# Kernel optimization log

Measured on AMD Instinct MI355X. Metric: run time of the kernel, lower is better.

## Reference

```python
import jax, jax.numpy as jnp
import numpy as np

WS = 16            # window height = width
DIM = 512          # channels
H = 16             # num heads
HD = DIM // H      # head dim = 32
NW = 64            # num windows per image (mask leading dim)
B_ = 256           # num_windows * batch
N_IN = 512         # pre-stride sequence length
SCALE = HD ** -0.5
MAX_SEQ = 512
STRIDE = 2


def _relative_position_index(wh, ww):
    coords = np.stack(np.meshgrid(np.arange(wh), np.arange(ww), indexing='ij'))  # (2, wh, ww)
    cf = coords.reshape(2, -1)                             # (2, wh*ww)
    rc = (cf[:, :, None] - cf[:, None, :]).transpose(1, 2, 0).astype(np.int32)
    rc[:, :, 0] += wh - 1
    rc[:, :, 1] += ww - 1
    rc[:, :, 0] *= 2 * ww - 1
    return rc.sum(-1)                                      # (wh*ww, wh*ww)


def setup_inputs() -> dict:
    key = jax.random.key(0)
    ks = jax.random.split(key, 8)
    x = jax.random.normal(ks[0], (B_, N_IN, DIM), dtype=jnp.float32)
    y = jax.random.normal(ks[1], (B_, N_IN, DIM), dtype=jnp.float32)
    mask = jax.random.normal(ks[2], (NW, WS * WS, WS * WS), dtype=jnp.float32)
    q_w = jax.random.normal(ks[3], (DIM, DIM), dtype=jnp.float32) * 0.02
    q_b = jnp.zeros((DIM,), dtype=jnp.float32)
    kv_w = jax.random.normal(ks[4], (2 * DIM, DIM), dtype=jnp.float32) * 0.02
    kv_b = jnp.zeros((2 * DIM,), dtype=jnp.float32)
    proj_w = jax.random.normal(ks[5], (DIM, DIM), dtype=jnp.float32) * 0.02
    proj_b = jnp.zeros((DIM,), dtype=jnp.float32)
    bias_table = jax.random.normal(ks[6], ((2 * WS - 1) ** 2, H), dtype=jnp.float32) * 0.02
    rel_pos_index = jnp.asarray(_relative_position_index(WS, WS))  # (256, 256) int32
    return {"x": x, "y": y, "mask": mask, "q_w": q_w, "q_b": q_b,
            "kv_w": kv_w, "kv_b": kv_b, "proj_w": proj_w, "proj_b": proj_b,
            "bias_table": bias_table, "rel_pos_index": rel_pos_index}


def reference(x, y, mask, q_w, q_b, kv_w, kv_b, proj_w, proj_b, bias_table, rel_pos_index):
    # truncate + stride (as in forward)
    x = x[:, :MAX_SEQ][:, ::STRIDE]          # (B_, N, C), N = 256
    y = y[:, :MAX_SEQ][:, ::STRIDE]
    b, n, c = x.shape
    # projections
    q = (x @ q_w.T + q_b).reshape(b, n, H, HD).transpose(0, 2, 1, 3)   # (B_, H, N, D)
    kv = y @ kv_w.T + kv_b                                              # (B_, N, 2C)
    k = kv[..., :DIM].reshape(b, n, H, HD).transpose(0, 2, 1, 3)
    v = kv[..., DIM:].reshape(b, n, H, HD).transpose(0, 2, 1, 3)
    # scores
    attn = jnp.einsum('bhnd,bhmd->bhnm', q * SCALE, k)                  # (B_, H, N, N)
    # gathered relative position bias: (N, N, H) -> (H, N, N)
    rpb = bias_table[rel_pos_index].transpose(2, 0, 1)
    attn = attn + rpb[None]
    # window mask: view (B_//nW, nW, H, N, N) + mask[None,:,None]
    attn = attn.reshape(b // NW, NW, H, n, n) + mask[None, :, None]
    attn = attn.reshape(b, H, n, n)
    attn = jax.nn.softmax(attn, axis=-1)
    out = jnp.einsum('bhnm,bhmd->bhnd', attn, v)                        # (B_, H, N, D)
    out = out.transpose(0, 2, 1, 3).reshape(b, n, DIM)
    out = out @ proj_w.T + proj_b
    return out
```

## Files before the change

kernel.cpp:

```cpp
#include <hip/hip_runtime.h>

typedef _Float16 half8 __attribute__((ext_vector_type(8)));
typedef _Float16 half4 __attribute__((ext_vector_type(4)));
typedef _Float16 half2v __attribute__((ext_vector_type(2)));
typedef float f32x4 __attribute__((ext_vector_type(4)));

#define LOG2E 1.4426950408889634f
#define QSCALE (0.17677669529663687f * 1.4426950408889634f)

static __device__ __forceinline__ half4 cvt4h(float4 v) {
    half2v a = __builtin_bit_cast(half2v, __builtin_amdgcn_cvt_pkrtz(v.x, v.y));
    half2v b = __builtin_bit_cast(half2v, __builtin_amdgcn_cvt_pkrtz(v.z, v.w));
    return half4{ a[0], a[1], b[0], b[1] };
}

static __device__ __forceinline__ void gl16(const _Float16* g, _Float16* l) {
    __builtin_amdgcn_global_load_lds(
        (const __attribute__((address_space(1))) void*)g,
        (__attribute__((address_space(3))) void*)l, 16, 0, 0);
}

#define NB_X 16384
#define NB_Y 16384
#define NB_W 512
#define NB_M 4096
#define NB_R 4096

__global__ __launch_bounds__(256) void convert_kernel(
    const float* __restrict__ x, const float* __restrict__ y,
    const float* __restrict__ q_w, const float* __restrict__ kv_w,
    const float* __restrict__ proj_w, const float* __restrict__ mask,
    const float* __restrict__ table, const int* __restrict__ rpi,
    _Float16* __restrict__ Xh, _Float16* __restrict__ Yh,
    _Float16* __restrict__ Wh, _Float16* __restrict__ maskh,
    _Float16* __restrict__ rpbh)
{
    const int blk = blockIdx.x, t = threadIdx.x;
    if (blk < NB_X + NB_Y) {
        const float* src; _Float16* dst; int v;
        if (blk < NB_X) { v = blk * 256 + t; src = x; dst = Xh; }
        else { v = (blk - NB_X) * 256 + t; src = y; dst = Yh; }
        int r = v >> 6, ks = (v & 63) * 8;
        const float* s = src + ((size_t)(r >> 8) * 512 + (size_t)((r & 255) * 2)) * 512 + ks;
        half4 h0 = cvt4h(*(const float4*)s);
        half4 h1 = cvt4h(*(const float4*)(s + 4));
        half8 hv = { h0[0], h0[1], h0[2], h0[3], h1[0], h1[1], h1[2], h1[3] };
        *(half8*)(dst + (size_t)v * 8) = hv;
    } else if (blk < NB_X + NB_Y + NB_W) {
        int v = (blk - NB_X - NB_Y) * 256 + t;
        int row = v >> 6, ks = (v & 63) * 8;
        const float* s; float sc = 1.0f;
        if (row < 512)       { s = q_w + (size_t)row * 512;            sc = QSCALE; }
        else if (row < 1536) { s = kv_w + (size_t)(row - 512) * 512; }
        else                 { s = proj_w + (size_t)(row - 1536) * 512; }
        float4 a = *(const float4*)(s + ks);
        float4 b = *(const float4*)(s + ks + 4);
        a.x *= sc; a.y *= sc; a.z *= sc; a.w *= sc;
        b.x *= sc; b.y *= sc; b.z *= sc; b.w *= sc;
        half4 h0 = cvt4h(a), h1 = cvt4h(b);
        half8 hv = { h0[0], h0[1], h0[2], h0[3], h1[0], h1[1], h1[2], h1[3] };
        *(half8*)(Wh + (size_t)v * 8) = hv;
    } else if (blk < NB_X + NB_Y + NB_W + NB_M) {
        int i = (blk - NB_X - NB_Y - NB_W) * 256 + t;
        float4 v = ((const float4*)mask)[i];
        half4 hv = { (_Float16)(v.x * LOG2E), (_Float16)(v.y * LOG2E),
                     (_Float16)(v.z * LOG2E), (_Float16)(v.w * LOG2E) };
        *(half4*)(maskh + (size_t)i * 4) = hv;
    } else {
        int i = (blk - NB_X - NB_Y - NB_W - NB_M) * 256 + t;
        int p = i & 65535, hh = i >> 16;
        rpbh[i] = (_Float16)(table[rpi[p] * 16 + hh] * LOG2E);
    }
}

__global__ __launch_bounds__(256) void gemm_f16(
    const _Float16* __restrict__ Ah, const _Float16* __restrict__ Wh,
    const float* __restrict__ bias, float bscale,
    _Float16* __restrict__ qout, _Float16* __restrict__ kout,
    _Float16* __restrict__ vout, float* __restrict__ fout,
    int mode, int nct_sh)
{
    __shared__ __align__(16) _Float16 As[128 * 64];
    __shared__ __align__(16) _Float16 Ws[128 * 64];
    const int nwg = gridDim.x;
    const int chunk = nwg >> 3;
    const int f = blockIdx.x;
    const int swz = (f & 7) * chunk + (f >> 3);
    const int ct = swz & ((1 << nct_sh) - 1);
    const int rt = swz >> nct_sh;

    const int t = threadIdx.x;
    const int lane = t & 63, wave = t >> 6;
    const int ql = lane & 15, g = lane >> 4;
    const int wr = (wave >> 1) * 64, wc = (wave & 1) * 64;

    const int lr = lane >> 3;
    const int ls = (lane & 7) ^ lr;
    const _Float16* aB = Ah + ((size_t)(rt * 128 + wave * 8 + lr)) * 512 + ls * 8;
    const _Float16* wB = Wh + ((size_t)(ct * 128 + wave * 8 + lr)) * 512 + ls * 8;
    _Float16* asW = As + wave * 8 * 64;
    _Float16* wsW = Ws + wave * 8 * 64;

    f32x4 acc[4][4] = {};
    for (int kk = 0; kk < 8; ++kk) {
        const int k0 = kk * 64;
        if (kk) __syncthreads();
#pragma unroll
        for (int p = 0; p < 4; ++p) {
            gl16(aB + (size_t)p * 32 * 512 + k0, asW + p * 32 * 64);
            gl16(wB + (size_t)p * 32 * 512 + k0, wsW + p * 32 * 64);
        }
        __syncthreads();
#pragma unroll
        for (int kh = 0; kh < 2; ++kh) {
            half8 af[4], bf[4];
#pragma unroll
            for (int i = 0; i < 4; ++i) {
                int row = wr + i * 16 + ql;
                af[i] = *(const half8*)((const char*)As + row * 128 +
                        (((kh * 4 + g) ^ (ql & 7)) << 4));
            }
#pragma unroll
            for (int j = 0; j < 4; ++j) {
                int row = wc + j * 16 + ql;
                bf[j] = *(const half8*)((const char*)Ws + row * 128 +
                        (((kh * 4 + g) ^ (ql & 7)) << 4));
            }
#pragma unroll
            for (int i = 0; i < 4; ++i)
#pragma unroll
                for (int j = 0; j < 4; ++j)
                    acc[i][j] = __builtin_amdgcn_mfma_f32_16x16x32_f16(af[i], bf[j], acc[i][j], 0, 0, 0);
        }
    }

#pragma unroll
    for (int j = 0; j < 4; ++j) {
        int c = ct * 128 + wc + j * 16 + ql;
        float bv = bias[c] * bscale;
#pragma unroll
        for (int i = 0; i < 4; ++i) {
#pragma unroll
            for (int rr = 0; rr < 4; ++rr) {
                int r = rt * 128 + wr + i * 16 + g * 4 + rr;
                float val = acc[i][j][rr] + bv;
                if (mode == 2) {
                    fout[(size_t)r * 512 + c] = val;
                } else {
                    _Float16 hv = (_Float16)val;
                    int b = r >> 8, n = r & 255;
                    if (mode == 0) {
                        int hh = c >> 5, d = c & 31;
                        qout[((size_t)(b * 16 + hh) * 256 + n) * 32 + d] = hv;
                    } else if (c < 512) {
                        int hh = c >> 5, d = c & 31;
                        kout[((size_t)(b * 16 + hh) * 256 + n) * 32 + d] = hv;
                    } else {
                        int c2 = c - 512, hh = c2 >> 5, d = c2 & 31;
                        vout[((size_t)(b * 16 + hh) * 256 + n) * 32 + d] = hv;
                    }
                }
            }
        }
    }
}

__global__ __launch_bounds__(256, 2) void attn_kernel(
    const _Float16* __restrict__ Q, const _Float16* __restrict__ K,
    const _Float16* __restrict__ V, const _Float16* __restrict__ rpbh,
    const _Float16* __restrict__ maskh, _Float16* __restrict__ pre)
{
    __shared__ __align__(16) _Float16 bias_s[2][16 * 256];
    const int blk = blockIdx.x;
    const int w = blk >> 4, h = blk & 15;
    const int t = threadIdx.x;
    const int lane = t & 63, wave = t >> 6;
    const int ql = lane & 15, g = lane >> 4;
    const int b = w + 64 * wave;
    const size_t blk_b = (size_t)(b * 16 + h) * 8192;
    const _Float16* Qp = Q + blk_b + g * 8;
    const _Float16* Kp = K + blk_b + ql * 32 + g * 8;
    const _Float16* rp = rpbh + (size_t)h * 65536;
    const _Float16* mp = maskh + (size_t)w * 65536;

    half8 karr[16];
#pragma unroll
    for (int tt = 0; tt < 16; ++tt)
        karr[tt] = *(const half8*)(Kp + tt * 512);

    half4 vf0[16], vf1[16];
    {
        const _Float16* vb = V + blk_b + g * 128 + ql;
#pragma unroll
        for (int tt = 0; tt < 16; ++tt) {
#pragma unroll
            for (int j = 0; j < 4; ++j) {
                vf0[tt][j] = vb[tt * 512 + j * 32];
                vf1[tt][j] = vb[tt * 512 + j * 32 + 16];
            }
        }
    }

    const int sq = t >> 4;
    const int scb = (t & 15) * 32;
    const int sw = sq << 3;
    const int sgoff = (t & 15) * 16;

    {
        const _Float16* rrow = rp + (size_t)sq * 256 + sgoff;
        const _Float16* mrow = mp + (size_t)sq * 256 + sgoff;
        half8 s0 = *(const half8*)rrow + *(const half8*)mrow;
        half8 s1 = *(const half8*)(rrow + 8) + *(const half8*)(mrow + 8);
        char* sb = (char*)bias_s[0] + sq * 512;
        *(half4*)(sb + ((scb) ^ sw))      = __builtin_shufflevector(s0, s0, 0, 1, 2, 3);
        *(half4*)(sb + ((scb + 8) ^ sw))  = __builtin_shufflevector(s0, s0, 4, 5, 6, 7);
        *(half4*)(sb + ((scb + 16) ^ sw)) = __builtin_shufflevector(s1, s1, 0, 1, 2, 3);
        *(half4*)(sb + ((scb + 24) ^ sw)) = __builtin_shufflevector(s1, s1, 4, 5, 6, 7);
    }
    __syncthreads();

#pragma unroll 1
    for (int qg = 0; qg < 16; ++qg) {
        const int q0 = qg * 16;
        half8 nr0, nm0, nr1, nm1;
        if (qg < 15) {
            const _Float16* rrow = rp + (size_t)(q0 + 16 + sq) * 256 + sgoff;
            const _Float16* mrow = mp + (size_t)(q0 + 16 + sq) * 256 + sgoff;
            nr0 = *(const half8*)rrow;
            nm0 = *(const half8*)mrow;
            nr1 = *(const half8*)(rrow + 8);
            nm1 = *(const half8*)(mrow + 8);
        }

        const int q = q0 + ql;
        half8 qf = *(const half8*)(Qp + (size_t)q * 32);
        const char* bb = (const char*)bias_s[qg & 1] + ql * 512;
        f32x4 lsum = { 0.f, 0.f, 0.f, 0.f };
        f32x4 o0 = { 0.f, 0.f, 0.f, 0.f }, o1 = { 0.f, 0.f, 0.f, 0.f };
#pragma unroll
        for (int tt = 0; tt < 16; ++tt) {
            half4 bs = *(const half4*)(bb + ((tt * 32 + g * 8) ^ (ql << 3)));
            f32x4 bf = { (float)bs[0], (float)bs[1], (float)bs[2], (float)bs[3] };
            f32x4 s = __builtin_amdgcn_mfma_f32_16x16x32_f16(karr[tt], qf, bf, 0, 0, 0);
            float e0 = __builtin_amdgcn_exp2f(s[0]);
            float e1 = __builtin_amdgcn_exp2f(s[1]);
            float e2 = __builtin_amdgcn_exp2f(s[2]);
            float e3 = __builtin_amdgcn_exp2f(s[3]);
            lsum[0] += e0; lsum[1] += e1; lsum[2] += e2; lsum[3] += e3;
            half2v p01 = __builtin_bit_cast(half2v, __builtin_amdgcn_cvt_pkrtz(e0, e1));
            half2v p23 = __builtin_bit_cast(half2v, __builtin_amdgcn_cvt_pkrtz(e2, e3));
            half4 pf = { p01[0], p01[1], p23[0], p23[1] };
            o0 = __builtin_amdgcn_mfma_f32_16x16x16f16(pf, vf0[tt], o0, 0, 0, 0);
            o1 = __builtin_amdgcn_mfma_f32_16x16x16f16(pf, vf1[tt], o1, 0, 0, 0);
        }
        float l = (lsum[0] + lsum[1]) + (lsum[2] + lsum[3]);
        l += __shfl_xor(l, 16);
        l += __shfl_xor(l, 32);
#pragma unroll
        for (int rr = 0; rr < 4; ++rr) {
            float inv = __builtin_amdgcn_rcpf(__shfl(l, g * 4 + rr));
            int row = q0 + g * 4 + rr;
            size_t ob = ((size_t)b * 256 + row) * 512 + h * 32;
            pre[ob + ql] = (_Float16)(o0[rr] * inv);
            pre[ob + 16 + ql] = (_Float16)(o1[rr] * inv);
        }
        if (qg < 15) {
            half8 s0 = nr0 + nm0, s1 = nr1 + nm1;
            char* sb = (char*)bias_s[(qg + 1) & 1] + sq * 512;
            *(half4*)(sb + ((scb) ^ sw))      = __builtin_shufflevector(s0, s0, 0, 1, 2, 3);
            *(half4*)(sb + ((scb + 8) ^ sw))  = __builtin_shufflevector(s0, s0, 4, 5, 6, 7);
            *(half4*)(sb + ((scb + 16) ^ sw)) = __builtin_shufflevector(s1, s1, 0, 1, 2, 3);
            *(half4*)(sb + ((scb + 24) ^ sw)) = __builtin_shufflevector(s1, s1, 4, 5, 6, 7);
        }
        __syncthreads();
    }
}

extern "C" void kernel_launch(void* const* d_in, const int* in_sizes, int n_in,
                              void* d_out, int out_size, void* d_ws, size_t ws_size,
                              hipStream_t stream)
{
    const float* x      = (const float*)d_in[0];
    const float* y      = (const float*)d_in[1];
    const float* mask   = (const float*)d_in[2];
    const float* q_w    = (const float*)d_in[3];
    const float* q_b    = (const float*)d_in[4];
    const float* kv_w   = (const float*)d_in[5];
    const float* kv_b   = (const float*)d_in[6];
    const float* proj_w = (const float*)d_in[7];
    const float* proj_b = (const float*)d_in[8];
    const float* btab   = (const float*)d_in[9];
    const int*   rpi    = (const int*)d_in[10];
    float* out = (float*)d_out;

    char* ws = (char*)d_ws;
    _Float16* XK  = (_Float16*)(ws);
    _Float16* YP  = (_Float16*)(ws + ((size_t)64 << 20));
    _Float16* Qw  = (_Float16*)(ws + ((size_t)128 << 20));
    _Float16* Vw  = (_Float16*)(ws + ((size_t)192 << 20));
    _Float16* Wh  = (_Float16*)(ws + ((size_t)256 << 20));
    _Float16* Rpb = (_Float16*)(ws + ((size_t)258 << 20));
    _Float16* Mh  = (_Float16*)(ws + ((size_t)260 << 20));

    convert_kernel<<<NB_X + NB_Y + NB_W + NB_M + NB_R, 256, 0, stream>>>(
        x, y, q_w, kv_w, proj_w, mask, btab, rpi, XK, YP, Wh, Mh, Rpb);
    gemm_f16<<<2048, 256, 0, stream>>>(XK, Wh, q_b, QSCALE,
                                       Qw, nullptr, nullptr, nullptr, 0, 2);
    gemm_f16<<<4096, 256, 0, stream>>>(YP, Wh + 512 * 512, kv_b, 1.0f,
                                       nullptr, XK, Vw, nullptr, 1, 3);
    attn_kernel<<<1024, 256, 0, stream>>>(Qw, XK, Vw, Rpb, Mh, YP);
    gemm_f16<<<2048, 256, 0, stream>>>(YP, Wh + 1536 * 512, proj_b, 1.0f,
                                       nullptr, nullptr, nullptr, out, 2, 2);
}
```

Measured before the change: 497.0 us.

## Fuse fp32-to-fp16 activation conversion into projection GEMM tile loads

Removes the standalone conversion pass over x and y and has the Q and KV projection GEMMs load fp32 strided rows directly, converting to fp16 in registers before storing to LDS. Global-to-LDS direct loads are replaced by a register-prefetch pipeline that loads the next K-slice while computing the current one. This removes an intermediate fp16 write and re-read, at the cost of reading wider fp32 data per column tile and more register pressure.

```diff
diff --git a/kernel.cpp b/kernel.cpp
--- a/kernel.cpp
+++ b/kernel.cpp
@@ -14,40 +14,20 @@
     return half4{ a[0], a[1], b[0], b[1] };
 }
 
-static __device__ __forceinline__ void gl16(const _Float16* g, _Float16* l) {
-    __builtin_amdgcn_global_load_lds(
-        (const __attribute__((address_space(1))) void*)g,
-        (__attribute__((address_space(3))) void*)l, 16, 0, 0);
-}
-
-#define NB_X 16384
-#define NB_Y 16384
-#define NB_W 512
-#define NB_M 4096
-#define NB_R 4096
-
-__global__ __launch_bounds__(256) void convert_kernel(
-    const float* __restrict__ x, const float* __restrict__ y,
+#define PB_W 512
+#define PB_M 4096
+#define PB_R 4096
+
+__global__ __launch_bounds__(256) void prep_kernel(
     const float* __restrict__ q_w, const float* __restrict__ kv_w,
     const float* __restrict__ proj_w, const float* __restrict__ mask,
     const float* __restrict__ table, const int* __restrict__ rpi,
-    _Float16* __restrict__ Xh, _Float16* __restrict__ Yh,
     _Float16* __restrict__ Wh, _Float16* __restrict__ maskh,
     _Float16* __restrict__ rpbh)
 {
     const int blk = blockIdx.x, t = threadIdx.x;
-    if (blk < NB_X + NB_Y) {
-        const float* src; _Float16* dst; int v;
-        if (blk < NB_X) { v = blk * 256 + t; src = x; dst = Xh; }
-        else { v = (blk - NB_X) * 256 + t; src = y; dst = Yh; }
-        int r = v >> 6, ks = (v & 63) * 8;
-        const float* s = src + ((size_t)(r >> 8) * 512 + (size_t)((r & 255) * 2)) * 512 + ks;
-        half4 h0 = cvt4h(*(const float4*)s);
-        half4 h1 = cvt4h(*(const float4*)(s + 4));
-        half8 hv = { h0[0], h0[1], h0[2], h0[3], h1[0], h1[1], h1[2], h1[3] };
-        *(half8*)(dst + (size_t)v * 8) = hv;
-    } else if (blk < NB_X + NB_Y + NB_W) {
-        int v = (blk - NB_X - NB_Y) * 256 + t;
+    if (blk < PB_W) {
+        int v = blk * 256 + t;
         int row = v >> 6, ks = (v & 63) * 8;
         const float* s; float sc = 1.0f;
         if (row < 512)       { s = q_w + (size_t)row * 512;            sc = QSCALE; }
@@ -60,23 +40,24 @@
         half4 h0 = cvt4h(a), h1 = cvt4h(b);
         half8 hv = { h0[0], h0[1], h0[2], h0[3], h1[0], h1[1], h1[2], h1[3] };
         *(half8*)(Wh + (size_t)v * 8) = hv;
-    } else if (blk < NB_X + NB_Y + NB_W + NB_M) {
-        int i = (blk - NB_X - NB_Y - NB_W) * 256 + t;
+    } else if (blk < PB_W + PB_M) {
+        int i = (blk - PB_W) * 256 + t;
         float4 v = ((const float4*)mask)[i];
         half4 hv = { (_Float16)(v.x * LOG2E), (_Float16)(v.y * LOG2E),
                      (_Float16)(v.z * LOG2E), (_Float16)(v.w * LOG2E) };
         *(half4*)(maskh + (size_t)i * 4) = hv;
     } else {
-        int i = (blk - NB_X - NB_Y - NB_W - NB_M) * 256 + t;
+        int i = (blk - PB_W - PB_M) * 256 + t;
         int p = i & 65535, hh = i >> 16;
         rpbh[i] = (_Float16)(table[rpi[p] * 16 + hh] * LOG2E);
     }
 }
 
-__global__ __launch_bounds__(256) void gemm_f16(
-    const _Float16* __restrict__ Ah, const _Float16* __restrict__ Wh,
-    const float* __restrict__ bias, float bscale,
-    _Float16* __restrict__ qout, _Float16* __restrict__ kout,
+template<bool F32A>
+static __device__ __forceinline__ void gemm_core(
+    const float* __restrict__ Af, const _Float16* __restrict__ Ah,
+    const _Float16* __restrict__ Wh, const float* __restrict__ bias,
+    float bscale, _Float16* __restrict__ qout, _Float16* __restrict__ kout,
     _Float16* __restrict__ vout, float* __restrict__ fout,
     int mode, int nct_sh)
 {
@@ -94,23 +75,64 @@
     const int ql = lane & 15, g = lane >> 4;
     const int wr = (wave >> 1) * 64, wc = (wave & 1) * 64;
 
-    const int lr = lane >> 3;
-    const int ls = (lane & 7) ^ lr;
-    const _Float16* aB = Ah + ((size_t)(rt * 128 + wave * 8 + lr)) * 512 + ls * 8;
-    const _Float16* wB = Wh + ((size_t)(ct * 128 + wave * 8 + lr)) * 512 + ls * 8;
-    _Float16* asW = As + wave * 8 * 64;
-    _Float16* wsW = Ws + wave * 8 * 64;
+    const int sr = t >> 3;
+    const int st = t & 7;
+    const float* aFp[4];
+    const _Float16* aHp[4];
+#pragma unroll
+    for (int p = 0; p < 4; ++p) {
+        int r = rt * 128 + sr + p * 32;
+        if constexpr (F32A)
+            aFp[p] = Af + ((size_t)(r >> 8) * 512 + (size_t)((r & 255) * 2)) * 512 + st * 8;
+        else
+            aHp[p] = Ah + (size_t)r * 512 + st * 8;
+    }
+    const _Float16* wR = Wh + ((size_t)(ct * 128 + sr)) * 512 + st * 8;
+    char* asw = (char*)As + sr * 128 + ((st ^ (sr & 7)) << 4);
+    char* wsw = (char*)Ws + sr * 128 + ((st ^ (sr & 7)) << 4);
+
+    float4 alo[4], ahi[4];
+    half8 aS[4], wS[4];
+#pragma unroll
+    for (int p = 0; p < 4; ++p) {
+        if constexpr (F32A) {
+            alo[p] = *(const float4*)(aFp[p]);
+            ahi[p] = *(const float4*)(aFp[p] + 4);
+        } else {
+            aS[p] = *(const half8*)(aHp[p]);
+        }
+        wS[p] = *(const half8*)(wR + p * 32 * 512);
+    }
 
     f32x4 acc[4][4] = {};
     for (int kk = 0; kk < 8; ++kk) {
-        const int k0 = kk * 64;
         if (kk) __syncthreads();
 #pragma unroll
         for (int p = 0; p < 4; ++p) {
-            gl16(aB + (size_t)p * 32 * 512 + k0, asW + p * 32 * 64);
-            gl16(wB + (size_t)p * 32 * 512 + k0, wsW + p * 32 * 64);
+            half8 av;
+            if constexpr (F32A) {
+                half4 l = cvt4h(alo[p]), h = cvt4h(ahi[p]);
+                av = half8{ l[0], l[1], l[2], l[3], h[0], h[1], h[2], h[3] };
+            } else {
+                av = aS[p];
+            }
+            *(half8*)(asw + p * 4096) = av;
+            *(half8*)(wsw + p * 4096) = wS[p];
         }
         __syncthreads();
+        if (kk < 7) {
+            const int k0n = (kk + 1) * 64;
+#pragma unroll
+            for (int p = 0; p < 4; ++p) {
+                if constexpr (F32A) {
+                    alo[p] = *(const float4*)(aFp[p] + k0n);
+                    ahi[p] = *(const float4*)(aFp[p] + k0n + 4);
+                } else {
+                    aS[p] = *(const half8*)(aHp[p] + k0n);
+                }
+                wS[p] = *(const half8*)(wR + p * 32 * 512 + k0n);
+            }
+        }
 #pragma unroll
         for (int kh = 0; kh < 2; ++kh) {
             half8 af[4], bf[4];
@@ -165,6 +187,24 @@
     }
 }
 
+__global__ __launch_bounds__(256) void gemm_f32a(
+    const float* __restrict__ Af, const _Float16* __restrict__ Wh,
+    const float* __restrict__ bias, float bscale,
+    _Float16* __restrict__ qout, _Float16* __restrict__ kout,
+    _Float16* __restrict__ vout, int mode, int nct_sh)
+{
+    gemm_core<true>(Af, nullptr, Wh, bias, bscale, qout, kout, vout,
+                    nullptr, mode, nct_sh);
+}
+
+__global__ __launch_bounds__(256) void gemm_f16a(
+    const _Float16* __restrict__ Ah, const _Float16* __restrict__ Wh,
+    const float* __restrict__ bias, float* __restrict__ fout, int nct_sh)
+{
+    gemm_core<false>(nullptr, Ah, Wh, bias, 1.0f, nullptr, nullptr, nullptr,
+                     fout, 2, nct_sh);
+}
+
 __global__ __launch_bounds__(256, 2) void attn_kernel(
     const _Float16* __restrict__ Q, const _Float16* __restrict__ K,
     const _Float16* __restrict__ V, const _Float16* __restrict__ rpbh,
@@ -294,21 +334,20 @@
     float* out = (float*)d_out;
 
     char* ws = (char*)d_ws;
-    _Float16* XK  = (_Float16*)(ws);
-    _Float16* YP  = (_Float16*)(ws + ((size_t)64 << 20));
-    _Float16* Qw  = (_Float16*)(ws + ((size_t)128 << 20));
-    _Float16* Vw  = (_Float16*)(ws + ((size_t)192 << 20));
+    _Float16* Qw  = (_Float16*)(ws);
+    _Float16* Kw  = (_Float16*)(ws + ((size_t)64 << 20));
+    _Float16* Vw  = (_Float16*)(ws + ((size_t)128 << 20));
+    _Float16* Pre = (_Float16*)(ws + ((size_t)192 << 20));
     _Float16* Wh  = (_Float16*)(ws + ((size_t)256 << 20));
     _Float16* Rpb = (_Float16*)(ws + ((size_t)258 << 20));
     _Float16* Mh  = (_Float16*)(ws + ((size_t)260 << 20));
 
-    convert_kernel<<<NB_X + NB_Y + NB_W + NB_M + NB_R, 256, 0, stream>>>(
-        x, y, q_w, kv_w, proj_w, mask, btab, rpi, XK, YP, Wh, Mh, Rpb);
-    gemm_f16<<<2048, 256, 0, stream>>>(XK, Wh, q_b, QSCALE,
-                                       Qw, nullptr, nullptr, nullptr, 0, 2);
-    gemm_f16<<<4096, 256, 0, stream>>>(YP, Wh + 512 * 512, kv_b, 1.0f,
-                                       nullptr, XK, Vw, nullptr, 1, 3);
-    attn_kernel<<<1024, 256, 0, stream>>>(Qw, XK, Vw, Rpb, Mh, YP);
-    gemm_f16<<<2048, 256, 0, stream>>>(YP, Wh + 1536 * 512, proj_b, 1.0f,
-                                       nullptr, nullptr, nullptr, out, 2, 2);
-}
+    prep_kernel<<<PB_W + PB_M + PB_R, 256, 0, stream>>>(
+        q_w, kv_w, proj_w, mask, btab, rpi, Wh, Mh, Rpb);
+    gemm_f32a<<<2048, 256, 0, stream>>>(x, Wh, q_b, QSCALE,
+                                        Qw, nullptr, nullptr, 0, 2);
+    gemm_f32a<<<4096, 256, 0, stream>>>(y, Wh + 512 * 512, kv_b, 1.0f,
+                                        nullptr, Kw, Vw, 1, 3);
+    attn_kernel<<<1024, 256, 0, stream>>>(Qw, Kw, Vw, Rpb, Mh, Pre);
+    gemm_f16a<<<2048, 256, 0, stream>>>(Pre, Wh + 1536 * 512, proj_b, out, 2);
+}
```

After: 484.5 us. 2.5% less time.

## Load GEMM operands directly from global memory into registers, dropping LDS staging

Applied to the files above, without the earlier changes.

The f16 GEMM no longer stages A and W tiles through shared memory with global_load_lds and two barriers per k-step. Each lane now reads its MFMA fragments straight from global memory, and the k-loop is fully unrolled. This removes LDS traffic and synchronization, but gives up the sharing of tiles between waves. Each A and W element is now fetched from global/L2 by two waves, and the reads are strided 16-byte loads that depend on cache hits.

```diff
diff --git a/kernel.cpp b/kernel.cpp
--- a/kernel.cpp
+++ b/kernel.cpp
@@ -12,12 +12,6 @@
     half2v a = __builtin_bit_cast(half2v, __builtin_amdgcn_cvt_pkrtz(v.x, v.y));
     half2v b = __builtin_bit_cast(half2v, __builtin_amdgcn_cvt_pkrtz(v.z, v.w));
     return half4{ a[0], a[1], b[0], b[1] };
-}
-
-static __device__ __forceinline__ void gl16(const _Float16* g, _Float16* l) {
-    __builtin_amdgcn_global_load_lds(
-        (const __attribute__((address_space(1))) void*)g,
-        (__attribute__((address_space(3))) void*)l, 16, 0, 0);
 }
 
 #define NB_X 16384
@@ -80,8 +74,6 @@
     _Float16* __restrict__ vout, float* __restrict__ fout,
     int mode, int nct_sh)
 {
-    __shared__ __align__(16) _Float16 As[128 * 64];
-    __shared__ __align__(16) _Float16 Ws[128 * 64];
     const int nwg = gridDim.x;
     const int chunk = nwg >> 3;
     const int f = blockIdx.x;
@@ -94,38 +86,22 @@
     const int ql = lane & 15, g = lane >> 4;
     const int wr = (wave >> 1) * 64, wc = (wave & 1) * 64;
 
-    const int lr = lane >> 3;
-    const int ls = (lane & 7) ^ lr;
-    const _Float16* aB = Ah + ((size_t)(rt * 128 + wave * 8 + lr)) * 512 + ls * 8;
-    const _Float16* wB = Wh + ((size_t)(ct * 128 + wave * 8 + lr)) * 512 + ls * 8;
-    _Float16* asW = As + wave * 8 * 64;
-    _Float16* wsW = Ws + wave * 8 * 64;
+    const _Float16* aB = Ah + ((size_t)(rt * 128 + wr + ql)) * 512 + g * 8;
+    const _Float16* wB = Wh + ((size_t)(ct * 128 + wc + ql)) * 512 + g * 8;
 
     f32x4 acc[4][4] = {};
+#pragma unroll
     for (int kk = 0; kk < 8; ++kk) {
-        const int k0 = kk * 64;
-        if (kk) __syncthreads();
-#pragma unroll
-        for (int p = 0; p < 4; ++p) {
-            gl16(aB + (size_t)p * 32 * 512 + k0, asW + p * 32 * 64);
-            gl16(wB + (size_t)p * 32 * 512 + k0, wsW + p * 32 * 64);
-        }
-        __syncthreads();
 #pragma unroll
         for (int kh = 0; kh < 2; ++kh) {
+            const int ko = kk * 64 + kh * 32;
             half8 af[4], bf[4];
 #pragma unroll
-            for (int i = 0; i < 4; ++i) {
-                int row = wr + i * 16 + ql;
-                af[i] = *(const half8*)((const char*)As + row * 128 +
-                        (((kh * 4 + g) ^ (ql & 7)) << 4));
-            }
-#pragma unroll
-            for (int j = 0; j < 4; ++j) {
-                int row = wc + j * 16 + ql;
-                bf[j] = *(const half8*)((const char*)Ws + row * 128 +
-                        (((kh * 4 + g) ^ (ql & 7)) << 4));
-            }
+            for (int i = 0; i < 4; ++i)
+                af[i] = *(const half8*)(aB + (size_t)i * 16 * 512 + ko);
+#pragma unroll
+            for (int j = 0; j < 4; ++j)
+                bf[j] = *(const half8*)(wB + (size_t)j * 16 * 512 + ko);
 #pragma unroll
             for (int i = 0; i < 4; ++i)
 #pragma unroll
```

Result: slower. 709.6 us (+42.8%).
